# Kernel optimization log

Hardware: AMD Instinct MI355X
Metric: run time of the kernel (lower is better)

## Reference

```python
import jax, jax.numpy as jnp
import numpy as np
from jax import lax

TF_ALPHA = 0.125


def _teacher_force(z, x, alpha):
    # z: (B, dz), x: (B, dx); force first dx dims of z where x is not NaN
    dx = x.shape[-1]
    head = z[:, :dx]
    forced = jnp.where(jnp.isnan(x), head, alpha * x + (1.0 - alpha) * head)
    return jnp.concatenate([forced, z[:, dx:]], axis=-1)


def setup_inputs() -> dict:
    key = jax.random.key(0)
    ks = jax.random.split(key, 8)
    B, T, dx, dz, dh, ds = 256, 1024, 64, 128, 512, 16
    X = jax.random.normal(ks[0], (B, T, dx), dtype=jnp.float32)
    inputs = jax.random.normal(ks[1], (B, T, ds), dtype=jnp.float32)
    # A in (0, 0.9) for stable linear part; small weight scales to avoid blowup over T steps
    A = jax.random.uniform(ks[2], (B, dz), dtype=jnp.float32) * 0.9
    W1 = jax.random.normal(ks[3], (B, dz, dh), dtype=jnp.float32) * (0.5 / np.sqrt(dh))
    W2 = jax.random.normal(ks[4], (B, dh, dz), dtype=jnp.float32) * (0.5 / np.sqrt(dz))
    h1 = jax.random.normal(ks[5], (B, dz), dtype=jnp.float32) * 0.1
    h2 = jax.random.normal(ks[6], (B, dh), dtype=jnp.float32) * 0.1
    C = jax.random.normal(ks[7], (B, dz, ds), dtype=jnp.float32) * (0.5 / np.sqrt(ds))
    return {"X": X, "inputs": inputs, "A": A, "W1": W1, "W2": W2,
            "h1": h1, "h2": h2, "C": C}


def _plrnn_forward(X, inputs, A, W1, W2, h1, h2, C):
    B, T, dx = X.shape
    dz = A.shape[-1]
    # z0 = zeros teacher-forced with alpha=1 from X[:, 0]
    z0 = jnp.zeros((B, dz), dtype=X.dtype)
    z0 = _teacher_force(z0, X[:, 0], alpha=1.0)

    Xt = jnp.transpose(X, (1, 0, 2))        # (T, B, dx)
    St = jnp.transpose(inputs, (1, 0, 2))   # (T, B, ds)

    def step(z, xs):
        x_t, s_t = xs
        zf = _teacher_force(z, x_t, TF_ALPHA)
        pre = jnp.einsum('bhz,bz->bh', W2, zf) + h2          # (B, dh)
        z_new = (A * zf
                 + jnp.einsum('bzh,bh->bz', W1, jax.nn.relu(pre))
                 + h1
                 + jnp.einsum('bzs,bs->bz', C, s_t))
        return z_new, z_new

    _, Z = lax.scan(step, z0, (Xt, St))      # Z: (T, B, dz)
    Z = jnp.transpose(Z, (1, 0, 2))          # (B, T, dz)
    return Z[:, :, :dx]                      # dim_x_proj == 0 path


def reference(X, inputs, A, W1, W2, h1, h2, C):
    return _plrnn_forward(X, inputs, A, W1, W2, h1, h2, C)
```

## Files before the change

kernel.cpp:

```cpp
#include <hip/hip_runtime.h>
#include <math.h>


#define NB 256
#define T  1024
#define DX 64
#define DZ 128
#define DH 512
#define DS 16
#define CHUNK 128

typedef _Float16 half8 __attribute__((ext_vector_type(8)));
typedef _Float16 v4h   __attribute__((ext_vector_type(4)));
typedef float    f32x4 __attribute__((ext_vector_type(4)));

__device__ __forceinline__ half8 cvt8(const float* __restrict__ src) {
  const float4 a = *reinterpret_cast<const float4*>(src);
  const float4 c = *reinterpret_cast<const float4*>(src + 4);
  half8 h;
  h[0] = (_Float16)a.x; h[1] = (_Float16)a.y; h[2] = (_Float16)a.z; h[3] = (_Float16)a.w;
  h[4] = (_Float16)c.x; h[5] = (_Float16)c.y; h[6] = (_Float16)c.z; h[7] = (_Float16)c.w;
  return h;
}

__device__ __forceinline__ f32x4 sel4(int c, f32x4 a, f32x4 b) {
  f32x4 r;
  r[0] = c ? a[0] : b[0];  r[1] = c ? a[1] : b[1];
  r[2] = c ? a[2] : b[2];  r[3] = c ? a[3] : b[3];
  return r;
}

template <int CTRL>
__device__ __forceinline__ float dpp_xor_add(float v) {
  const int t = __builtin_amdgcn_update_dpp(0, __float_as_int(v), CTRL, 0xF, 0xF, true);
  return v + __int_as_float(t);
}

__global__ __launch_bounds__(512, 2) void plrnn_kernel(
    const float* __restrict__ X, const float* __restrict__ S,
    const float* __restrict__ A, const float* __restrict__ W1,
    const float* __restrict__ W2, const float* __restrict__ h1,
    const float* __restrict__ h2, const float* __restrict__ C,
    float* __restrict__ out)
{
  __shared__ __align__(16) _Float16 zf_h[DZ];
  __shared__ __align__(16) _Float16 rt[544];
  __shared__ __align__(16) float    part[DZ][9];
  __shared__ __align__(16) float    Xc[CHUNK][DX];
  __shared__ __align__(16) float    Sc[CHUNK][DS];
  __shared__ __align__(16) float    outc[CHUNK][DX];

  const int b    = blockIdx.x;
  const int tid  = threadIdx.x;
  const int w    = tid >> 6;
  const int l    = tid & 63;
  const int g    = l >> 4;
  const int r15  = l & 15;
  const int c4   = l & 3;
  const int k16  = l >> 2;
  const int row0 = 16 * w + k16;

  {
    #pragma unroll
    for (int k = 0; k < 4; ++k) {
      const int flat = k * 2048 + tid * 4;
      int srow = 1 + (flat >> 6);
      if (srow > T - 1) srow = T - 1;
      const float4 v = *reinterpret_cast<const float4*>(X + ((size_t)b * T + srow) * DX + (flat & 63));
      *reinterpret_cast<float4*>(&((float*)Xc)[flat]) = v;
    }
    const int flat = tid * 4;
    const float4 v = *reinterpret_cast<const float4*>(S + ((size_t)b * T) * DS + flat);
    *reinterpret_cast<float4*>(&((float*)Sc)[flat]) = v;
  }

  if (tid < 16) {
    rt[512 + tid] = (_Float16)S[((size_t)b * T) * DS + tid];
    rt[528 + tid] = (_Float16)0.0f;
  }

  half8 w2f[4][4];
  #pragma unroll
  for (int mt = 0; mt < 4; ++mt)
    #pragma unroll
    for (int kt = 0; kt < 4; ++kt)
      w2f[mt][kt] = cvt8(W2 + ((size_t)b * DH + 64 * w + 16 * mt + r15) * DZ + 32 * kt + 8 * g);

  half8 w1f[8][2];
  #pragma unroll
  for (int mt = 0; mt < 8; ++mt)
    #pragma unroll
    for (int kt = 0; kt < 2; ++kt)
      w1f[mt][kt] = cvt8(W1 + ((size_t)b * DZ + 16 * mt + r15) * DH + 64 * w + 32 * kt + 8 * g);

  half8 w1ft;
  #pragma unroll
  for (int e = 0; e < 8; ++e) w1ft[e] = (_Float16)0.0f;
  {
    const int row = 16 * w + r15;
    if (g == 0)      w1ft = cvt8(C + ((size_t)b * DZ + row) * DS + 0);
    else if (g == 1) w1ft = cvt8(C + ((size_t)b * DZ + row) * DS + 8);
  }

  f32x4 h2v[4];
  #pragma unroll
  for (int mt = 0; mt < 4; ++mt)
    h2v[mt] = *reinterpret_cast<const f32x4*>(h2 + (size_t)b * DH + 64 * w + 16 * mt + 4 * g);

  const float Areg  = A[(size_t)b * DZ + row0];
  const float h1reg = h1[(size_t)b * DZ + row0];
  float zfcur = 0.f;
  if (row0 < DX) {
    const float x0 = X[((size_t)b * T) * DX + row0];
    zfcur = (x0 != x0) ? 0.f : x0;
  }
  if (c4 == 0) zf_h[row0] = (_Float16)zfcur;
  __syncthreads();

  const f32x4 zero4 = {0.f, 0.f, 0.f, 0.f};

  for (int t = 0; t < T; ++t) {
    if ((t & (CHUNK - 1)) == 0 && t) {
      const int c0 = t - CHUNK;
      #pragma unroll
      for (int k = 0; k < 4; ++k) {
        const int flat = k * 2048 + tid * 4;
        const float4 v = *reinterpret_cast<const float4*>(&((float*)outc)[flat]);
        *reinterpret_cast<float4*>(out + ((size_t)b * T + c0) * DX + flat) = v;
      }
      #pragma unroll
      for (int k = 0; k < 4; ++k) {
        const int flat = k * 2048 + tid * 4;
        int srow = t + 1 + (flat >> 6);
        if (srow > T - 1) srow = T - 1;
        const float4 v = *reinterpret_cast<const float4*>(X + ((size_t)b * T + srow) * DX + (flat & 63));
        *reinterpret_cast<float4*>(&((float*)Xc)[flat]) = v;
      }
      {
        const int flat = tid * 4;
        const float4 v = *reinterpret_cast<const float4*>(S + ((size_t)b * T + t) * DS + flat);
        *reinterpret_cast<float4*>(&((float*)Sc)[flat]) = v;
      }
      if (tid < 16) rt[512 + tid] = (_Float16)S[((size_t)b * T + t) * DS + tid];
      __syncthreads();
    }
    const int tc = t & (CHUNK - 1);

    half8 bz[4];
    #pragma unroll
    for (int kt = 0; kt < 4; ++kt)
      bz[kt] = *reinterpret_cast<const half8*>(zf_h + 32 * kt + 8 * g);

    f32x4 acc1[4];
    #pragma unroll
    for (int mt = 0; mt < 4; ++mt)
      acc1[mt] = __builtin_amdgcn_mfma_f32_16x16x32_f16(w2f[mt][0], bz[0], h2v[mt], 0, 0, 0);
    #pragma unroll
    for (int kt = 1; kt < 4; ++kt)
      #pragma unroll
      for (int mt = 0; mt < 4; ++mt)
        acc1[mt] = __builtin_amdgcn_mfma_f32_16x16x32_f16(w2f[mt][kt], bz[kt], acc1[mt], 0, 0, 0);

    {
      const f32x4 s01 = sel4(r15 & 1, acc1[1], acc1[0]);
      const f32x4 s23 = sel4(r15 & 1, acc1[3], acc1[2]);
      const f32x4 sv  = sel4(r15 & 2, s23, s01);
      if (r15 < 4) {
        v4h p;
        p[0] = (_Float16)fmaxf(sv[0], 0.f);
        p[1] = (_Float16)fmaxf(sv[1], 0.f);
        p[2] = (_Float16)fmaxf(sv[2], 0.f);
        p[3] = (_Float16)fmaxf(sv[3], 0.f);
        *reinterpret_cast<v4h*>(&rt[64 * w + 16 * r15 + 4 * g]) = p;
      }
    }

    const half8 brt = *reinterpret_cast<const half8*>(rt + 512 + 8 * g);
    const half8 br0 = *reinterpret_cast<const half8*>(rt + 64 * w + 8 * g);
    const half8 br1 = *reinterpret_cast<const half8*>(rt + 64 * w + 32 + 8 * g);

    const f32x4 tailv = __builtin_amdgcn_mfma_f32_16x16x32_f16(w1ft, brt, zero4, 0, 0, 0);

    f32x4 acc2[8];
    #pragma unroll
    for (int mt = 0; mt < 8; ++mt)
      acc2[mt] = __builtin_amdgcn_mfma_f32_16x16x32_f16(w1f[mt][0], br0,
                                                        (mt == w) ? tailv : zero4, 0, 0, 0);
    #pragma unroll
    for (int mt = 0; mt < 8; ++mt)
      acc2[mt] = __builtin_amdgcn_mfma_f32_16x16x32_f16(w1f[mt][1], br1, acc2[mt], 0, 0, 0);

    {
      const int jp = r15 >> 3;
      float e0[8], e1[8];
      #pragma unroll
      for (int mt = 0; mt < 8; ++mt) {
        e0[mt] = jp ? acc2[mt][2] : acc2[mt][0];
        e1[mt] = jp ? acc2[mt][3] : acc2[mt][1];
      }
      const int m0 = r15 & 1, m1 = r15 & 2, m2 = r15 & 4;
      const float q0a = m0 ? e0[1] : e0[0], q0b = m0 ? e0[3] : e0[2];
      const float q0c = m0 ? e0[5] : e0[4], q0d = m0 ? e0[7] : e0[6];
      const float q1a = m0 ? e1[1] : e1[0], q1b = m0 ? e1[3] : e1[2];
      const float q1c = m0 ? e1[5] : e1[4], q1d = m0 ? e1[7] : e1[6];
      const float r0a = m1 ? q0b : q0a, r0b = m1 ? q0d : q0c;
      const float r1a = m1 ? q1b : q1a, r1b = m1 ? q1d : q1c;
      const float v0  = m2 ? r0b : r0a;
      const float v1  = m2 ? r1b : r1a;
      const int z0 = 16 * (r15 & 7) + 4 * g + 2 * jp;
      part[z0][w]     = v0;
      part[z0 + 1][w] = v1;
    }
    __syncthreads();

    float u = part[row0][c4] + part[row0][4 + c4];
    u = dpp_xor_add<0xB1>(u);
    u = dpp_xor_add<0x4E>(u);

    const float zn = Areg * zfcur + u + h1reg;
    float zfn = zn;
    if (row0 < DX) {
      const float x = Xc[tc][row0];
      zfn = (x != x) ? zn : (0.125f * x + 0.875f * zn);
      if (c4 == 0) outc[tc][row0] = zn;
    }
    zfcur = zfn;
    if (c4 == 0) zf_h[row0] = (_Float16)zfn;

    if (w == 7 && l < 4 && ((t + 1) & (CHUNK - 1)) != 0) {
      const f32x4 sv = *reinterpret_cast<const f32x4*>(&Sc[(t + 1) & (CHUNK - 1)][4 * l]);
      v4h sp;
      #pragma unroll
      for (int j = 0; j < 4; ++j) sp[j] = (_Float16)sv[j];
      *reinterpret_cast<v4h*>(&rt[512 + 4 * l]) = sp;
    }
    __syncthreads();
  }

  {
    const int c0 = T - CHUNK;
    #pragma unroll
    for (int k = 0; k < 4; ++k) {
      const int flat = k * 2048 + tid * 4;
      const float4 v = *reinterpret_cast<const float4*>(&((float*)outc)[flat]);
      *reinterpret_cast<float4*>(out + ((size_t)b * T + c0) * DX + flat) = v;
    }
  }
}

extern "C" void kernel_launch(void* const* d_in, const int* in_sizes, int n_in,
                              void* d_out, int out_size, void* d_ws, size_t ws_size,
                              hipStream_t stream) {
  const float* X  = (const float*)d_in[0];
  const float* S  = (const float*)d_in[1];
  const float* A  = (const float*)d_in[2];
  const float* W1 = (const float*)d_in[3];
  const float* W2 = (const float*)d_in[4];
  const float* h1 = (const float*)d_in[5];
  const float* h2 = (const float*)d_in[6];
  const float* C  = (const float*)d_in[7];
  float* out = (float*)d_out;
  plrnn_kernel<<<dim3(NB), dim3(512), 0, stream>>>(X, S, A, W1, W2, h1, h2, C, out);
}
```

Before: 1.130 ms.

## Split recurrent step across 16 waves and fold input projection into reduction

Doubles the block to 1024 threads, so each wave owns 32 hidden units. This halves the per-wave W2/W1 MFMA chain in each sequential timestep. The cross-wave reduction widens to 16 partial columns in a padded, rotated shared buffer, summed with an extra DPP stage. The C·s input term and h1 bias move from a dedicated MFMA into scalar FMAs in that reduction. The cost is more waves meeting at each barrier, h2 added from an f16 copy, and a tight register budget from the new launch bounds that may cause spills.

```diff
diff --git a/kernel.cpp b/kernel.cpp
--- a/kernel.cpp
+++ b/kernel.cpp
@@ -9,6 +9,7 @@
 #define DH 512
 #define DS 16
 #define CHUNK 128
+#define PSTR 17
 
 typedef _Float16 half8 __attribute__((ext_vector_type(8)));
 typedef _Float16 v4h   __attribute__((ext_vector_type(4)));
@@ -23,6 +24,12 @@
   return h;
 }
 
+template <int CTRL>
+__device__ __forceinline__ float dpp_add(float v) {
+  const int t = __builtin_amdgcn_update_dpp(0, __float_as_int(v), CTRL, 0xF, 0xF, true);
+  return v + __int_as_float(t);
+}
+
 __device__ __forceinline__ f32x4 sel4(int c, f32x4 a, f32x4 b) {
   f32x4 r;
   r[0] = c ? a[0] : b[0];  r[1] = c ? a[1] : b[1];
@@ -30,13 +37,7 @@
   return r;
 }
 
-template <int CTRL>
-__device__ __forceinline__ float dpp_xor_add(float v) {
-  const int t = __builtin_amdgcn_update_dpp(0, __float_as_int(v), CTRL, 0xF, 0xF, true);
-  return v + __int_as_float(t);
-}
-
-__global__ __launch_bounds__(512, 2) void plrnn_kernel(
+__global__ __launch_bounds__(1024, 4) void plrnn_kernel(
     const float* __restrict__ X, const float* __restrict__ S,
     const float* __restrict__ A, const float* __restrict__ W1,
     const float* __restrict__ W2, const float* __restrict__ h1,
@@ -44,8 +45,8 @@
     float* __restrict__ out)
 {
   __shared__ __align__(16) _Float16 zf_h[DZ];
-  __shared__ __align__(16) _Float16 rt[544];
-  __shared__ __align__(16) float    part[DZ][9];
+  __shared__ __align__(16) _Float16 rt[DH];
+  __shared__ __align__(16) float    part[DZ * PSTR];
   __shared__ __align__(16) float    Xc[CHUNK][DX];
   __shared__ __align__(16) float    Sc[CHUNK][DS];
   __shared__ __align__(16) float    outc[CHUNK][DX];
@@ -56,65 +57,57 @@
   const int l    = tid & 63;
   const int g    = l >> 4;
   const int r15  = l & 15;
-  const int c4   = l & 3;
-  const int k16  = l >> 2;
-  const int row0 = 16 * w + k16;
+  const int i8   = l & 7;
+  const int row0 = 8 * w + (l >> 3);
+  const int m    = r15 & 7;
+  const int jp   = r15 >> 3;
 
   {
     #pragma unroll
-    for (int k = 0; k < 4; ++k) {
-      const int flat = k * 2048 + tid * 4;
+    for (int k = 0; k < 2; ++k) {
+      const int flat = k * 4096 + tid * 4;
       int srow = 1 + (flat >> 6);
       if (srow > T - 1) srow = T - 1;
       const float4 v = *reinterpret_cast<const float4*>(X + ((size_t)b * T + srow) * DX + (flat & 63));
       *reinterpret_cast<float4*>(&((float*)Xc)[flat]) = v;
     }
-    const int flat = tid * 4;
-    const float4 v = *reinterpret_cast<const float4*>(S + ((size_t)b * T) * DS + flat);
-    *reinterpret_cast<float4*>(&((float*)Sc)[flat]) = v;
-  }
-
-  if (tid < 16) {
-    rt[512 + tid] = (_Float16)S[((size_t)b * T) * DS + tid];
-    rt[528 + tid] = (_Float16)0.0f;
-  }
-
-  half8 w2f[4][4];
+    if (tid < 512) {
+      const int flat = tid * 4;
+      const float4 v = *reinterpret_cast<const float4*>(S + ((size_t)b * T) * DS + flat);
+      *reinterpret_cast<float4*>(&((float*)Sc)[flat]) = v;
+    }
+  }
+
+  half8 w2f[2][4];
   #pragma unroll
-  for (int mt = 0; mt < 4; ++mt)
+  for (int mt = 0; mt < 2; ++mt)
     #pragma unroll
     for (int kt = 0; kt < 4; ++kt)
-      w2f[mt][kt] = cvt8(W2 + ((size_t)b * DH + 64 * w + 16 * mt + r15) * DZ + 32 * kt + 8 * g);
-
-  half8 w1f[8][2];
+      w2f[mt][kt] = cvt8(W2 + ((size_t)b * DH + 32 * w + 16 * mt + r15) * DZ + 32 * kt + 8 * g);
+
+  half8 w1f[8];
   #pragma unroll
   for (int mt = 0; mt < 8; ++mt)
-    #pragma unroll
-    for (int kt = 0; kt < 2; ++kt)
-      w1f[mt][kt] = cvt8(W1 + ((size_t)b * DZ + 16 * mt + r15) * DH + 64 * w + 32 * kt + 8 * g);
-
-  half8 w1ft;
+    w1f[mt] = cvt8(W1 + ((size_t)b * DZ + 16 * mt + r15) * DH + 32 * w + 8 * g);
+
+  v4h h2pk[2];
   #pragma unroll
-  for (int e = 0; e < 8; ++e) w1ft[e] = (_Float16)0.0f;
-  {
-    const int row = 16 * w + r15;
-    if (g == 0)      w1ft = cvt8(C + ((size_t)b * DZ + row) * DS + 0);
-    else if (g == 1) w1ft = cvt8(C + ((size_t)b * DZ + row) * DS + 8);
-  }
-
-  f32x4 h2v[4];
-  #pragma unroll
-  for (int mt = 0; mt < 4; ++mt)
-    h2v[mt] = *reinterpret_cast<const f32x4*>(h2 + (size_t)b * DH + 64 * w + 16 * mt + 4 * g);
+  for (int mt = 0; mt < 2; ++mt) {
+    const f32x4 hv = *reinterpret_cast<const f32x4*>(h2 + (size_t)b * DH + 32 * w + 16 * mt + 4 * g);
+    #pragma unroll
+    for (int j = 0; j < 4; ++j) h2pk[mt][j] = (_Float16)hv[j];
+  }
 
   const float Areg  = A[(size_t)b * DZ + row0];
   const float h1reg = h1[(size_t)b * DZ + row0];
+  const float Cp0   = C[((size_t)b * DZ + row0) * DS + 2 * i8];
+  const float Cp1   = C[((size_t)b * DZ + row0) * DS + 2 * i8 + 1];
   float zfcur = 0.f;
   if (row0 < DX) {
     const float x0 = X[((size_t)b * T) * DX + row0];
     zfcur = (x0 != x0) ? 0.f : x0;
   }
-  if (c4 == 0) zf_h[row0] = (_Float16)zfcur;
+  if (i8 == 0) zf_h[row0] = (_Float16)zfcur;
   __syncthreads();
 
   const f32x4 zero4 = {0.f, 0.f, 0.f, 0.f};
@@ -123,25 +116,24 @@
     if ((t & (CHUNK - 1)) == 0 && t) {
       const int c0 = t - CHUNK;
       #pragma unroll
-      for (int k = 0; k < 4; ++k) {
-        const int flat = k * 2048 + tid * 4;
+      for (int k = 0; k < 2; ++k) {
+        const int flat = k * 4096 + tid * 4;
         const float4 v = *reinterpret_cast<const float4*>(&((float*)outc)[flat]);
         *reinterpret_cast<float4*>(out + ((size_t)b * T + c0) * DX + flat) = v;
       }
       #pragma unroll
-      for (int k = 0; k < 4; ++k) {
-        const int flat = k * 2048 + tid * 4;
+      for (int k = 0; k < 2; ++k) {
+        const int flat = k * 4096 + tid * 4;
         int srow = t + 1 + (flat >> 6);
         if (srow > T - 1) srow = T - 1;
         const float4 v = *reinterpret_cast<const float4*>(X + ((size_t)b * T + srow) * DX + (flat & 63));
         *reinterpret_cast<float4*>(&((float*)Xc)[flat]) = v;
       }
-      {
+      if (tid < 512) {
         const int flat = tid * 4;
         const float4 v = *reinterpret_cast<const float4*>(S + ((size_t)b * T + t) * DS + flat);
         *reinterpret_cast<float4*>(&((float*)Sc)[flat]) = v;
       }
-      if (tid < 16) rt[512 + tid] = (_Float16)S[((size_t)b * T + t) * DS + tid];
       __syncthreads();
     }
     const int tc = t & (CHUNK - 1);
@@ -151,97 +143,75 @@
     for (int kt = 0; kt < 4; ++kt)
       bz[kt] = *reinterpret_cast<const half8*>(zf_h + 32 * kt + 8 * g);
 
-    f32x4 acc1[4];
-    #pragma unroll
-    for (int mt = 0; mt < 4; ++mt)
-      acc1[mt] = __builtin_amdgcn_mfma_f32_16x16x32_f16(w2f[mt][0], bz[0], h2v[mt], 0, 0, 0);
+    f32x4 acc1[2];
+    #pragma unroll
+    for (int mt = 0; mt < 2; ++mt)
+      acc1[mt] = __builtin_amdgcn_mfma_f32_16x16x32_f16(w2f[mt][0], bz[0], zero4, 0, 0, 0);
     #pragma unroll
     for (int kt = 1; kt < 4; ++kt)
       #pragma unroll
-      for (int mt = 0; mt < 4; ++mt)
+      for (int mt = 0; mt < 2; ++mt)
         acc1[mt] = __builtin_amdgcn_mfma_f32_16x16x32_f16(w2f[mt][kt], bz[kt], acc1[mt], 0, 0, 0);
 
+    if (r15 == 0) {
+      #pragma unroll
+      for (int mt = 0; mt < 2; ++mt) {
+        v4h p;
+        #pragma unroll
+        for (int j = 0; j < 4; ++j)
+          p[j] = (_Float16)fmaxf(acc1[mt][j] + (float)h2pk[mt][j], 0.f);
+        *reinterpret_cast<v4h*>(&rt[32 * w + 16 * mt + 4 * g]) = p;
+      }
+    }
+
+    const half8 br = *reinterpret_cast<const half8*>(rt + 32 * w + 8 * g);
+    f32x4 acc2[8];
+    #pragma unroll
+    for (int mt = 0; mt < 8; ++mt)
+      acc2[mt] = __builtin_amdgcn_mfma_f32_16x16x32_f16(w1f[mt], br, zero4, 0, 0, 0);
+
     {
-      const f32x4 s01 = sel4(r15 & 1, acc1[1], acc1[0]);
-      const f32x4 s23 = sel4(r15 & 1, acc1[3], acc1[2]);
-      const f32x4 sv  = sel4(r15 & 2, s23, s01);
-      if (r15 < 4) {
-        v4h p;
-        p[0] = (_Float16)fmaxf(sv[0], 0.f);
-        p[1] = (_Float16)fmaxf(sv[1], 0.f);
-        p[2] = (_Float16)fmaxf(sv[2], 0.f);
-        p[3] = (_Float16)fmaxf(sv[3], 0.f);
-        *reinterpret_cast<v4h*>(&rt[64 * w + 16 * r15 + 4 * g]) = p;
-      }
-    }
-
-    const half8 brt = *reinterpret_cast<const half8*>(rt + 512 + 8 * g);
-    const half8 br0 = *reinterpret_cast<const half8*>(rt + 64 * w + 8 * g);
-    const half8 br1 = *reinterpret_cast<const half8*>(rt + 64 * w + 32 + 8 * g);
-
-    const f32x4 tailv = __builtin_amdgcn_mfma_f32_16x16x32_f16(w1ft, brt, zero4, 0, 0, 0);
-
-    f32x4 acc2[8];
-    #pragma unroll
-    for (int mt = 0; mt < 8; ++mt)
-      acc2[mt] = __builtin_amdgcn_mfma_f32_16x16x32_f16(w1f[mt][0], br0,
-                                                        (mt == w) ? tailv : zero4, 0, 0, 0);
-    #pragma unroll
-    for (int mt = 0; mt < 8; ++mt)
-      acc2[mt] = __builtin_amdgcn_mfma_f32_16x16x32_f16(w1f[mt][1], br1, acc2[mt], 0, 0, 0);
-
-    {
-      const int jp = r15 >> 3;
-      float e0[8], e1[8];
-      #pragma unroll
-      for (int mt = 0; mt < 8; ++mt) {
-        e0[mt] = jp ? acc2[mt][2] : acc2[mt][0];
-        e1[mt] = jp ? acc2[mt][3] : acc2[mt][1];
-      }
-      const int m0 = r15 & 1, m1 = r15 & 2, m2 = r15 & 4;
-      const float q0a = m0 ? e0[1] : e0[0], q0b = m0 ? e0[3] : e0[2];
-      const float q0c = m0 ? e0[5] : e0[4], q0d = m0 ? e0[7] : e0[6];
-      const float q1a = m0 ? e1[1] : e1[0], q1b = m0 ? e1[3] : e1[2];
-      const float q1c = m0 ? e1[5] : e1[4], q1d = m0 ? e1[7] : e1[6];
-      const float r0a = m1 ? q0b : q0a, r0b = m1 ? q0d : q0c;
-      const float r1a = m1 ? q1b : q1a, r1b = m1 ? q1d : q1c;
-      const float v0  = m2 ? r0b : r0a;
-      const float v1  = m2 ? r1b : r1a;
-      const int z0 = 16 * (r15 & 7) + 4 * g + 2 * jp;
-      part[z0][w]     = v0;
-      part[z0 + 1][w] = v1;
+      const f32x4 s01 = sel4(r15 & 1, acc2[1], acc2[0]);
+      const f32x4 s23 = sel4(r15 & 1, acc2[3], acc2[2]);
+      const f32x4 s45 = sel4(r15 & 1, acc2[5], acc2[4]);
+      const f32x4 s67 = sel4(r15 & 1, acc2[7], acc2[6]);
+      const f32x4 a03 = sel4(r15 & 2, s23, s01);
+      const f32x4 a47 = sel4(r15 & 2, s67, s45);
+      const f32x4 q   = sel4(r15 & 4, a47, a03);
+      const float v1  = jp ? q[1] : q[0];
+      const float v2  = jp ? q[3] : q[2];
+      const int z1 = 16 * m + 4 * g + jp;
+      const int z2 = z1 + 2;
+      part[z1 * PSTR + ((w + (z1 >> 5)) & 15)] = v1;
+      part[z2 * PSTR + ((w + (z2 >> 5)) & 15)] = v2;
     }
     __syncthreads();
 
-    float u = part[row0][c4] + part[row0][4 + c4];
-    u = dpp_xor_add<0xB1>(u);
-    u = dpp_xor_add<0x4E>(u);
-
-    const float zn = Areg * zfcur + u + h1reg;
+    const float p0 = part[row0 * PSTR + 2 * i8];
+    const float p1 = part[row0 * PSTR + 2 * i8 + 1];
+    const float2 s2 = *reinterpret_cast<const float2*>(&Sc[tc][2 * i8]);
+    float u = p0 + p1 + Cp0 * s2.x + Cp1 * s2.y + ((i8 == 0) ? h1reg : 0.f);
+    u = dpp_add<0xB1>(u);
+    u = dpp_add<0x4E>(u);
+    u = dpp_add<0x141>(u);
+
+    const float zn = Areg * zfcur + u;
     float zfn = zn;
-    if (row0 < DX) {
+    if (w < 8) {
       const float x = Xc[tc][row0];
       zfn = (x != x) ? zn : (0.125f * x + 0.875f * zn);
-      if (c4 == 0) outc[tc][row0] = zn;
+      if (i8 == 0) outc[tc][row0] = zn;
     }
     zfcur = zfn;
-    if (c4 == 0) zf_h[row0] = (_Float16)zfn;
-
-    if (w == 7 && l < 4 && ((t + 1) & (CHUNK - 1)) != 0) {
-      const f32x4 sv = *reinterpret_cast<const f32x4*>(&Sc[(t + 1) & (CHUNK - 1)][4 * l]);
-      v4h sp;
-      #pragma unroll
-      for (int j = 0; j < 4; ++j) sp[j] = (_Float16)sv[j];
-      *reinterpret_cast<v4h*>(&rt[512 + 4 * l]) = sp;
-    }
+    if (i8 == 0) zf_h[row0] = (_Float16)zfn;
     __syncthreads();
   }
 
   {
     const int c0 = T - CHUNK;
     #pragma unroll
-    for (int k = 0; k < 4; ++k) {
-      const int flat = k * 2048 + tid * 4;
+    for (int k = 0; k < 2; ++k) {
+      const int flat = k * 4096 + tid * 4;
       const float4 v = *reinterpret_cast<const float4*>(&((float*)outc)[flat]);
       *reinterpret_cast<float4*>(out + ((size_t)b * T + c0) * DX + flat) = v;
     }
@@ -260,5 +230,5 @@
   const float* h2 = (const float*)d_in[6];
   const float* C  = (const float*)d_in[7];
   float* out = (float*)d_out;
-  plrnn_kernel<<<dim3(NB), dim3(512), 0, stream>>>(X, S, A, W1, W2, h1, h2, C, out);
-}
+  plrnn_kernel<<<dim3(NB), dim3(1024), 0, stream>>>(X, S, A, W1, W2, h1, h2, C, out);
+}
```

New measurement: 1.131 ms. No clear change (+0.1%).
